# Kernel tuning notes

Measured on AMD Instinct MI355X. Metric: run time of the kernel, lower is better.

Reference implementation:

```python
import jax, jax.numpy as jnp
import numpy as np


def setup_inputs() -> dict:
    key = jax.random.key(0)
    ks = jax.random.split(key, 4)
    B, T, IN, H, OUT = 256, 128, 128, 256, 128
    s = 0.05  # small init scale to keep gates unsaturated
    return {
        "x": jax.random.normal(ks[0], (B, T, IN), dtype=jnp.float32),
        "hid_state": jnp.zeros((1, 3, B, H), dtype=jnp.float32),
        "Wx": jax.random.normal(ks[1], (IN, 3 * H), dtype=jnp.float32) * s,
        "bx": jnp.zeros((3 * H,), dtype=jnp.float32),
        "Wh": jax.random.normal(ks[2], (H, 3 * H), dtype=jnp.float32) * s,
        "bh": jnp.zeros((3 * H,), dtype=jnp.float32),
        "Wf": jax.random.normal(ks[3], (H, OUT), dtype=jnp.float32) * s,
        "bf": jnp.zeros((OUT,), dtype=jnp.float32),
    }


def reference(x, hid_state, Wx, bx, Wh, bh, Wf, bf):
    # x: (B, T, IN); hid_state: (num_layers=1, 3, B, H)
    h0 = hid_state[0]  # (3, B, H) three-component CRU hidden state

    def step(h, xt):
        gx = xt @ Wx + bx                      # (B, 3H)
        gh = h @ Wh + bh                       # (3, B, 3H)
        ir, iz, inn = jnp.split(gx, 3, axis=-1)
        hr, hz, hn = jnp.split(gh, 3, axis=-1)
        r = jax.nn.sigmoid(ir[None] + hr)      # (3, B, H)
        z = jax.nn.sigmoid(iz[None] + hz)
        n = jnp.tanh(inn[None] + r * hn)
        h_new = n + z * (h - n)                # GRU-style update, (3, B, H)
        return h_new, None

    hT, _ = jax.lax.scan(step, h0, jnp.swapaxes(x, 0, 1))  # scan over T
    feature = jnp.mean(hT, axis=1)                          # (3, H): mean over batch
    out = jnp.sum(hT, axis=0)                               # (B, H): sum over components
    out = jax.nn.elu(out @ Wf + bf)                         # (B, OUT)
    return out, feature
```

## Files before the change

kernel.cpp:

```cpp
#include <hip/hip_runtime.h>

#define B_   256
#define T_   128
#define IN_  128
#define H_   256
#define H3_  768
#define OUT_ 128

#define L2E  1.4426950408889634f

typedef unsigned short u16;
typedef u16   u16x4  __attribute__((ext_vector_type(4)));
typedef u16   u16x8  __attribute__((ext_vector_type(8)));
typedef __bf16 bf16x8 __attribute__((ext_vector_type(8)));
typedef float f32x4  __attribute__((ext_vector_type(4)));
typedef int   i32x4  __attribute__((ext_vector_type(4)));
typedef signed char c8x8 __attribute__((ext_vector_type(8)));

__device__ __forceinline__ float bf2f(u16 u) {
  unsigned int v = ((unsigned int)u) << 16;
  return __builtin_bit_cast(float, v);
}
__device__ __forceinline__ u16 f2bf(float f) {
  unsigned int u = __builtin_bit_cast(unsigned int, f);
  u += 0x7fffu + ((u >> 16) & 1u);
  return (u16)(u >> 16);
}
__device__ __forceinline__ f32x4 mfma16(bf16x8 a, bf16x8 b, f32x4 c) {
  return __builtin_amdgcn_mfma_f32_16x16x32_bf16(a, b, c, 0, 0, 0);
}
__device__ __forceinline__ i32x4 mfma8(i32x4 a, i32x4 b, i32x4 c) {
  return __builtin_amdgcn_mfma_i32_16x16x64_i8(a, b, c, 0, 0, 0);
}
__device__ __forceinline__ float exp2f_(float x) {
#if __has_builtin(__builtin_amdgcn_exp2f)
  return __builtin_amdgcn_exp2f(x);
#else
  return __builtin_exp2f(x);
#endif
}
__device__ __forceinline__ float rcp_(float x) { return __builtin_amdgcn_rcpf(x); }

__device__ __forceinline__ int pick4i(i32x4 v, int e) {
  int r = v[0];
  r = (e == 1) ? v[1] : r;
  r = (e == 2) ? v[2] : r;
  r = (e == 3) ? v[3] : r;
  return r;
}

__global__ __launch_bounds__(1024) void prep0(const float* __restrict__ Wx,
                                              const float* __restrict__ Wh,
                                              u16* __restrict__ WxT,
                                              float* __restrict__ sw) {
  const int bid = blockIdx.x;
  if (bid < 96) {
    int o = bid * 1024 + threadIdx.x;
    int n = o >> 7, k = o & 127;
    WxT[o] = f2bf(Wx[(size_t)k * H3_ + n]);
  } else {
    __shared__ float red[16][64];
    const int n0 = (bid - 96) * 64;
    const int nl = threadIdx.x & 63, kg = threadIdx.x >> 6;
    float m = 1e-30f;
    #pragma unroll
    for (int i = 0; i < 16; ++i)
      m = fmaxf(m, fabsf(Wh[(size_t)(kg * 16 + i) * H3_ + n0 + nl]));
    red[kg][nl] = m;
    __syncthreads();
    if (threadIdx.x < 64) {
      float v = m;
      #pragma unroll
      for (int i = 1; i < 16; ++i) v = fmaxf(v, red[i][nl]);
      sw[n0 + nl] = v * (1.f / 127.f);
    }
  }
}

__global__ __launch_bounds__(512) void prep1(const float* __restrict__ x,
                                             const u16* __restrict__ WxT,
                                             const float* __restrict__ bx,
                                             const float* __restrict__ bh,
                                             const float* __restrict__ Wh,
                                             const float* __restrict__ sw,
                                             u16* __restrict__ gxw,
                                             signed char* __restrict__ whp8) {
  __shared__ __align__(16) char smem[(128 * 136 + 384 * 136) * 2];
  const int bid = blockIdx.x;
  const int tid = threadIdx.x;

  if (bid < 48) {
    int o8 = bid * 512 + tid;
    int j8 = o8 & 1;
    int kk = (o8 >> 1) & 3;
    int g  = (o8 >> 3) % 3;
    int tp = o8 / 24;
    int l  = tp & 63, w = tp >> 6;
    int n  = g * 256 + w * 16 + (l & 15);
    int kbase = kk * 64 + ((l >> 4) & 3) * 16 + j8 * 8;
    float rs = rcp_(sw[n]);
    c8x8 v;
    #pragma unroll
    for (int j = 0; j < 8; ++j) {
      float q = __builtin_rintf(Wh[(size_t)(kbase + j) * H3_ + n] * rs);
      v[j] = (signed char)(int)q;
    }
    *(c8x8*)(whp8 + (size_t)o8 * 8) = v;
    return;
  }

  u16 (*As)[136] = (u16(*)[136])smem;
  u16 (*Bs)[136] = (u16(*)[136])(smem + 128 * 136 * 2);
  u16 (*St)[392] = (u16(*)[392])smem;

  const int gb = bid - 48;
  const int mt = gb & 255;
  const int n0 = (gb >> 8) * 384;
  const int m0 = mt * 128;
  const int t  = mt >> 1;
  const int brow0 = (mt & 1) * 128;
  const int w = tid >> 6, lane = tid & 63, quad = lane >> 4, r = lane & 15;
  const int wm = w >> 2, wn = w & 3;

  {
    int row = tid >> 2;
    int colc = (tid & 3) * 4;
    const float* s = x + ((size_t)(brow0 + row) * T_ + t) * IN_ + colc;
    #pragma unroll
    for (int c4 = 0; c4 < 8; ++c4) {
      f32x4 v = *(const f32x4*)(s + c4 * 16);
      u16x4 b;
      b[0] = f2bf(v[0]); b[1] = f2bf(v[1]); b[2] = f2bf(v[2]); b[3] = f2bf(v[3]);
      *(u16x4*)&As[row][colc + c4 * 16] = b;
    }
  }
  {
    #pragma unroll
    for (int i = 0; i < 12; ++i) {
      int idx = tid + i * 512;
      int row = idx >> 4, col8 = (idx & 15) * 8;
      *(u16x8*)&Bs[row][col8] = *(const u16x8*)(WxT + (size_t)(n0 + row) * IN_ + col8);
    }
  }
  __syncthreads();

  f32x4 acc[4][6];
  #pragma unroll
  for (int i = 0; i < 4; ++i)
    #pragma unroll
    for (int j = 0; j < 6; ++j)
      acc[i][j] = (f32x4){0.f, 0.f, 0.f, 0.f};

  #pragma unroll
  for (int kk = 0; kk < 4; ++kk) {
    bf16x8 a[4];
    #pragma unroll
    for (int m2 = 0; m2 < 4; ++m2)
      a[m2] = *(const bf16x8*)&As[wm * 64 + m2 * 16 + r][kk * 32 + quad * 8];
    #pragma unroll
    for (int n2 = 0; n2 < 6; ++n2) {
      bf16x8 b = *(const bf16x8*)&Bs[wn * 96 + n2 * 16 + r][kk * 32 + quad * 8];
      #pragma unroll
      for (int m2 = 0; m2 < 4; ++m2)
        acc[m2][n2] = mfma16(a[m2], b, acc[m2][n2]);
    }
  }

  __syncthreads();

  #pragma unroll
  for (int m2 = 0; m2 < 4; ++m2)
    #pragma unroll
    for (int n2 = 0; n2 < 6; ++n2) {
      int nl = wn * 96 + n2 * 16 + r;
      int n  = n0 + nl;
      float sc = (n < 512) ? L2E : (2.f * L2E);
      float bias = bx[n] + (n < 512 ? bh[n] : 0.f);
      #pragma unroll
      for (int e = 0; e < 4; ++e) {
        int mrow = wm * 64 + m2 * 16 + quad * 4 + e;
        St[mrow][nl] = f2bf((acc[m2][n2][e] + bias) * sc);
      }
    }
  __syncthreads();

  #pragma unroll
  for (int i = 0; i < 12; ++i) {
    int idx = tid + i * 512;
    int row = idx / 48, c8 = (idx % 48) * 8;
    *(u16x8*)(gxw + (size_t)(m0 + row) * H3_ + n0 + c8) = *(const u16x8*)&St[row][c8];
  }
}

__global__ __launch_bounds__(1024)
void cru_scan(const float* __restrict__ hid,
              const signed char* __restrict__ whp8,
              const float* __restrict__ sw,
              const float* __restrict__ bh,
              const u16*  __restrict__ gx,
              float* __restrict__ hT) {
  __shared__ __align__(16) signed char h8[2][4][288];

  const int bid = blockIdx.x;
  const int c   = bid >> 6;
  const int b0  = (bid & 63) << 2;
  const int tid = threadIdx.x;
  const int lane = tid & 63, quad = lane >> 4, m = lane & 15;
  const int w  = tid >> 6;
  const int bb = m & 3;
  const int e  = m >> 2;
  const int hcol = w * 16 + quad * 4 + e;

  i32x4 bfr[3][4];
  {
    const signed char* wp = whp8 + (size_t)tid * 192;
    #pragma unroll
    for (int g = 0; g < 3; ++g)
      #pragma unroll
      for (int kk = 0; kk < 4; ++kk)
        bfr[g][kk] = *(const i32x4*)(wp + g * 64 + kk * 16);
  }

  const float dqR = sw[hcol]       * (L2E / 127.f);
  const float dqZ = sw[256 + hcol] * (L2E / 127.f);
  const float dqN = sw[512 + hcol] * (2.f * L2E / 127.f);

  const size_t hrow = (size_t)(c * 256 + b0 + bb) * 256 + hcol;
  float hx = hid[hrow];
  h8[0][bb][hcol] = (signed char)(int)__builtin_rintf(fminf(fmaxf(hx, -1.f), 1.f) * 127.f);
  const float bn0 = bh[512 + hcol] * (2.f * L2E);

  const u16* gxp = gx + (size_t)(b0 + bb) * H3_ + hcol;
  const int rbase = bb * 288 + quad * 16;

  u16 xr = gxp[0], xz = gxp[256], xn = gxp[512];
  const u16* gxs = gxp + (size_t)(B_ * H3_);

  __syncthreads();

  #pragma unroll 2
  for (int t = 0; t < T_; ++t) {
    const int sel = t & 1;

    const signed char* hb = &h8[sel][0][0];
    i32x4 f0 = *(const i32x4*)(hb + rbase);
    i32x4 f1 = *(const i32x4*)(hb + rbase + 64);
    i32x4 f2 = *(const i32x4*)(hb + rbase + 128);
    i32x4 f3 = *(const i32x4*)(hb + rbase + 192);

    __builtin_amdgcn_s_setprio(1);
    i32x4 accR = {0, 0, 0, 0};
    i32x4 accZ = {0, 0, 0, 0};
    i32x4 accN = {0, 0, 0, 0};
    accR = mfma8(bfr[0][0], f0, accR);
    accZ = mfma8(bfr[1][0], f0, accZ);
    accN = mfma8(bfr[2][0], f0, accN);
    accR = mfma8(bfr[0][1], f1, accR);
    accZ = mfma8(bfr[1][1], f1, accZ);
    accN = mfma8(bfr[2][1], f1, accN);
    accR = mfma8(bfr[0][2], f2, accR);
    accZ = mfma8(bfr[1][2], f2, accZ);
    accN = mfma8(bfr[2][2], f2, accN);
    accR = mfma8(bfr[0][3], f3, accR);
    accZ = mfma8(bfr[1][3], f3, accZ);
    accN = mfma8(bfr[2][3], f3, accN);
    __builtin_amdgcn_s_setprio(0);

    u16 nxr = gxs[0], nxz = gxs[256], nxn = gxs[512];
    gxs += B_ * H3_;

    float gR = (float)pick4i(accR, e) * dqR;
    float gZ = (float)pick4i(accZ, e) * dqZ;
    float sr = rcp_(1.f + exp2f_(-(bf2f(xr) + gR)));
    float sz = rcp_(1.f + exp2f_(-(bf2f(xz) + gZ)));

    float gN = (float)pick4i(accN, e) * dqN;
    float nv = bf2f(xn) + sr * (gN + bn0);
    float nn = fmaf(2.f, rcp_(1.f + exp2f_(-nv)), -1.f);
    float hv = nn + sz * (hx - nn);
    hx = hv;
    h8[sel ^ 1][bb][hcol] = (signed char)(int)__builtin_rintf(hv * 127.f);
    xr = nxr; xz = nxz; xn = nxn;
    __syncthreads();
  }

  hT[hrow] = hx;
}

__global__ __launch_bounds__(128) void finalize(const float* __restrict__ hT,
                                                const float* __restrict__ Wf,
                                                const float* __restrict__ bfv,
                                                float* __restrict__ out) {
  __shared__ float hsum[256];
  const int bid = blockIdx.x, tid = threadIdx.x;
  if (bid < 256) {
    const int b = bid;
    for (int k = tid; k < 256; k += 128)
      hsum[k] = hT[((size_t)(0 * 256 + b)) * 256 + k]
              + hT[((size_t)(1 * 256 + b)) * 256 + k]
              + hT[((size_t)(2 * 256 + b)) * 256 + k];
    __syncthreads();
    float acc = bfv[tid];
    #pragma unroll 8
    for (int k = 0; k < 256; ++k)
      acc = fmaf(hsum[k], Wf[(size_t)k * OUT_ + tid], acc);
    float rv = acc > 0.f ? acc : (__expf(acc) - 1.f);
    out[b * OUT_ + tid] = rv;
  } else {
    const int idx = bid - 256;
    const int c = idx >> 1, j = ((idx & 1) << 7) + tid;
    float sum = 0.f;
    #pragma unroll 4
    for (int b = 0; b < 256; ++b)
      sum += hT[((size_t)(c * 256 + b)) * 256 + j];
    out[B_ * OUT_ + c * 256 + j] = sum * (1.f / 256.f);
  }
}

extern "C" void kernel_launch(void* const* d_in, const int* in_sizes, int n_in,
                              void* d_out, int out_size, void* d_ws, size_t ws_size,
                              hipStream_t stream) {
  const float* x   = (const float*)d_in[0];
  const float* hid = (const float*)d_in[1];
  const float* Wx  = (const float*)d_in[2];
  const float* bx  = (const float*)d_in[3];
  const float* Wh  = (const float*)d_in[4];
  const float* bh  = (const float*)d_in[5];
  const float* Wf  = (const float*)d_in[6];
  const float* bf_ = (const float*)d_in[7];
  float* out = (float*)d_out;

  char* ws = (char*)d_ws;
  u16* WxT   = (u16*)ws;
  u16* gxw   = (u16*)(ws + (1 << 18));
  size_t off = (1 << 18) + (size_t)T_ * B_ * H3_ * 2;
  float* hTw = (float*)(ws + off);
  off += (size_t)3 * 256 * 256 * 4;
  signed char* whp8 = (signed char*)(ws + off);
  off += (size_t)1024 * 192;
  float* sww = (float*)(ws + off);

  prep0<<<108, 1024, 0, stream>>>(Wx, Wh, WxT, sww);
  prep1<<<560, 512, 0, stream>>>(x, WxT, bx, bh, Wh, sww, gxw, whp8);
  cru_scan<<<192, 1024, 0, stream>>>(hid, whp8, sww, bh, gxw, hTw);
  finalize<<<262, 128, 0, stream>>>(hTw, Wf, bf_, out);
}
```

Measured before the change: 194.5 us.

## Halve scan block size, give each wave two 16-column hidden tiles

The recurrent scan kernel now runs 512 threads per block instead of 1024. Each wave covers 32 hidden columns with two sets of int8 MFMA accumulators and two gate updates, and the packed weight layout in prep1 is reordered to match. The goal is to make the per-step block barrier cheaper with fewer waves and to raise per-wave instruction-level parallelism by interleaving independent MFMA chains. In exchange each thread holds twice the weight registers (96 VGPRs of B fragments) and does twice the serial elementwise gate work per step.

New measurement: 204.6 us. +5.2%, slower.

```diff
diff --git a/kernel.cpp b/kernel.cpp
--- a/kernel.cpp
+++ b/kernel.cpp
@@ -91,12 +91,14 @@
 
   if (bid < 48) {
     int o8 = bid * 512 + tid;
-    int j8 = o8 & 1;
-    int kk = (o8 >> 1) & 3;
-    int g  = (o8 >> 3) % 3;
-    int tp = o8 / 24;
+    int tp  = o8 / 48;
+    int idx = o8 % 48;
+    int g  = idx >> 4;
+    int s  = (idx >> 3) & 1;
+    int kk = (idx >> 1) & 3;
+    int j8 = idx & 1;
     int l  = tp & 63, w = tp >> 6;
-    int n  = g * 256 + w * 16 + (l & 15);
+    int n  = g * 256 + w * 32 + s * 16 + (l & 15);
     int kbase = kk * 64 + ((l >> 4) & 3) * 16 + j8 * 8;
     float rs = rcp_(sw[n]);
     c8x8 v;
@@ -192,7 +194,7 @@
   }
 }
 
-__global__ __launch_bounds__(1024)
+__global__ __launch_bounds__(512)
 void cru_scan(const float* __restrict__ hid,
               const signed char* __restrict__ whp8,
               const float* __restrict__ sw,
@@ -209,31 +211,42 @@
   const int w  = tid >> 6;
   const int bb = m & 3;
   const int e  = m >> 2;
-  const int hcol = w * 16 + quad * 4 + e;
-
-  i32x4 bfr[3][4];
+  const int hcol0 = w * 32 + quad * 4 + e;
+  const int hcol1 = hcol0 + 16;
+
+  i32x4 bfr[3][2][4];
   {
-    const signed char* wp = whp8 + (size_t)tid * 192;
+    const signed char* wp = whp8 + (size_t)tid * 384;
     #pragma unroll
     for (int g = 0; g < 3; ++g)
       #pragma unroll
-      for (int kk = 0; kk < 4; ++kk)
-        bfr[g][kk] = *(const i32x4*)(wp + g * 64 + kk * 16);
-  }
-
-  const float dqR = sw[hcol]       * (L2E / 127.f);
-  const float dqZ = sw[256 + hcol] * (L2E / 127.f);
-  const float dqN = sw[512 + hcol] * (2.f * L2E / 127.f);
-
-  const size_t hrow = (size_t)(c * 256 + b0 + bb) * 256 + hcol;
-  float hx = hid[hrow];
-  h8[0][bb][hcol] = (signed char)(int)__builtin_rintf(fminf(fmaxf(hx, -1.f), 1.f) * 127.f);
-  const float bn0 = bh[512 + hcol] * (2.f * L2E);
-
-  const u16* gxp = gx + (size_t)(b0 + bb) * H3_ + hcol;
+      for (int s = 0; s < 2; ++s)
+        #pragma unroll
+        for (int kk = 0; kk < 4; ++kk)
+          bfr[g][s][kk] = *(const i32x4*)(wp + g * 128 + s * 64 + kk * 16);
+  }
+
+  const float dqR0 = sw[hcol0]       * (L2E / 127.f);
+  const float dqR1 = sw[hcol1]       * (L2E / 127.f);
+  const float dqZ0 = sw[256 + hcol0] * (L2E / 127.f);
+  const float dqZ1 = sw[256 + hcol1] * (L2E / 127.f);
+  const float dqN0 = sw[512 + hcol0] * (2.f * L2E / 127.f);
+  const float dqN1 = sw[512 + hcol1] * (2.f * L2E / 127.f);
+
+  const size_t hrow0 = (size_t)(c * 256 + b0 + bb) * 256 + hcol0;
+  float hx0 = hid[hrow0];
+  float hx1 = hid[hrow0 + 16];
+  h8[0][bb][hcol0] = (signed char)(int)__builtin_rintf(fminf(fmaxf(hx0, -1.f), 1.f) * 127.f);
+  h8[0][bb][hcol1] = (signed char)(int)__builtin_rintf(fminf(fmaxf(hx1, -1.f), 1.f) * 127.f);
+  const float bn0 = bh[512 + hcol0] * (2.f * L2E);
+  const float bn1 = bh[512 + hcol1] * (2.f * L2E);
+
+  const u16* gxp = gx + (size_t)(b0 + bb) * H3_ + hcol0;
   const int rbase = bb * 288 + quad * 16;
 
-  u16 xr = gxp[0], xz = gxp[256], xn = gxp[512];
+  u16 xr0 = gxp[0],   xr1 = gxp[16];
+  u16 xz0 = gxp[256], xz1 = gxp[272];
+  u16 xn0 = gxp[512], xn1 = gxp[528];
   const u16* gxs = gxp + (size_t)(B_ * H3_);
 
   __syncthreads();
@@ -249,42 +262,58 @@
     i32x4 f3 = *(const i32x4*)(hb + rbase + 192);
 
     __builtin_amdgcn_s_setprio(1);
-    i32x4 accR = {0, 0, 0, 0};
-    i32x4 accZ = {0, 0, 0, 0};
-    i32x4 accN = {0, 0, 0, 0};
-    accR = mfma8(bfr[0][0], f0, accR);
-    accZ = mfma8(bfr[1][0], f0, accZ);
-    accN = mfma8(bfr[2][0], f0, accN);
-    accR = mfma8(bfr[0][1], f1, accR);
-    accZ = mfma8(bfr[1][1], f1, accZ);
-    accN = mfma8(bfr[2][1], f1, accN);
-    accR = mfma8(bfr[0][2], f2, accR);
-    accZ = mfma8(bfr[1][2], f2, accZ);
-    accN = mfma8(bfr[2][2], f2, accN);
-    accR = mfma8(bfr[0][3], f3, accR);
-    accZ = mfma8(bfr[1][3], f3, accZ);
-    accN = mfma8(bfr[2][3], f3, accN);
+    i32x4 aR0 = {0,0,0,0}, aR1 = {0,0,0,0};
+    i32x4 aZ0 = {0,0,0,0}, aZ1 = {0,0,0,0};
+    i32x4 aN0 = {0,0,0,0}, aN1 = {0,0,0,0};
+#define STEP_(kk, fk) \
+    aR0 = mfma8(bfr[0][0][kk], fk, aR0); \
+    aR1 = mfma8(bfr[0][1][kk], fk, aR1); \
+    aZ0 = mfma8(bfr[1][0][kk], fk, aZ0); \
+    aZ1 = mfma8(bfr[1][1][kk], fk, aZ1); \
+    aN0 = mfma8(bfr[2][0][kk], fk, aN0); \
+    aN1 = mfma8(bfr[2][1][kk], fk, aN1);
+    STEP_(0, f0)
+    STEP_(1, f1)
+    STEP_(2, f2)
+    STEP_(3, f3)
+#undef STEP_
     __builtin_amdgcn_s_setprio(0);
 
-    u16 nxr = gxs[0], nxz = gxs[256], nxn = gxs[512];
+    u16 nr0 = gxs[0],   nr1 = gxs[16];
+    u16 nz0 = gxs[256], nz1 = gxs[272];
+    u16 nn0_ = gxs[512], nn1_ = gxs[528];
     gxs += B_ * H3_;
 
-    float gR = (float)pick4i(accR, e) * dqR;
-    float gZ = (float)pick4i(accZ, e) * dqZ;
-    float sr = rcp_(1.f + exp2f_(-(bf2f(xr) + gR)));
-    float sz = rcp_(1.f + exp2f_(-(bf2f(xz) + gZ)));
-
-    float gN = (float)pick4i(accN, e) * dqN;
-    float nv = bf2f(xn) + sr * (gN + bn0);
-    float nn = fmaf(2.f, rcp_(1.f + exp2f_(-nv)), -1.f);
-    float hv = nn + sz * (hx - nn);
-    hx = hv;
-    h8[sel ^ 1][bb][hcol] = (signed char)(int)__builtin_rintf(hv * 127.f);
-    xr = nxr; xz = nxz; xn = nxn;
+    {
+      float gR = (float)pick4i(aR0, e) * dqR0;
+      float gZ = (float)pick4i(aZ0, e) * dqZ0;
+      float sr = rcp_(1.f + exp2f_(-(bf2f(xr0) + gR)));
+      float sz = rcp_(1.f + exp2f_(-(bf2f(xz0) + gZ)));
+      float gN = (float)pick4i(aN0, e) * dqN0;
+      float nv = bf2f(xn0) + sr * (gN + bn0);
+      float nn = fmaf(2.f, rcp_(1.f + exp2f_(-nv)), -1.f);
+      float hv = nn + sz * (hx0 - nn);
+      hx0 = hv;
+      h8[sel ^ 1][bb][hcol0] = (signed char)(int)__builtin_rintf(hv * 127.f);
+    }
+    {
+      float gR = (float)pick4i(aR1, e) * dqR1;
+      float gZ = (float)pick4i(aZ1, e) * dqZ1;
+      float sr = rcp_(1.f + exp2f_(-(bf2f(xr1) + gR)));
+      float sz = rcp_(1.f + exp2f_(-(bf2f(xz1) + gZ)));
+      float gN = (float)pick4i(aN1, e) * dqN1;
+      float nv = bf2f(xn1) + sr * (gN + bn1);
+      float nn = fmaf(2.f, rcp_(1.f + exp2f_(-nv)), -1.f);
+      float hv = nn + sz * (hx1 - nn);
+      hx1 = hv;
+      h8[sel ^ 1][bb][hcol1] = (signed char)(int)__builtin_rintf(hv * 127.f);
+    }
+    xr0 = nr0; xr1 = nr1; xz0 = nz0; xz1 = nz1; xn0 = nn0_; xn1 = nn1_;
     __syncthreads();
   }
 
-  hT[hrow] = hx;
+  hT[hrow0] = hx0;
+  hT[hrow0 + 16] = hx1;
 }
 
 __global__ __launch_bounds__(128) void finalize(const float* __restrict__ hT,
@@ -337,11 +366,11 @@
   float* hTw = (float*)(ws + off);
   off += (size_t)3 * 256 * 256 * 4;
   signed char* whp8 = (signed char*)(ws + off);
-  off += (size_t)1024 * 192;
+  off += (size_t)512 * 384;
   float* sww = (float*)(ws + off);
 
   prep0<<<108, 1024, 0, stream>>>(Wx, Wh, WxT, sww);
   prep1<<<560, 512, 0, stream>>>(x, WxT, bx, bh, Wh, sww, gxw, whp8);
-  cru_scan<<<192, 1024, 0, stream>>>(hid, whp8, sww, bh, gxw, hTw);
+  cru_scan<<<192, 512, 0, stream>>>(hid, whp8, sww, bh, gxw, hTw);
   finalize<<<262, 128, 0, stream>>>(hTw, Wf, bf_, out);
 }
```
